# Kernel tuning notes

Hardware: AMD Instinct MI355X
Metric: run time of the kernel (lower is better)

Reference implementation:

```python
import jax, jax.numpy as jnp
import numpy as np

H = 4      # attention heads in HGTConv
DH = 32    # head dim
D = 128    # hidden size (rnn.hidden_size == hidden_size)
PAD = 0    # pad_idx


def setup_inputs() -> dict:
    key = jax.random.key(0)
    ks = jax.random.split(key, 16)
    Na = Np = 50000
    E = 800000
    V = 10000
    L = 8
    s = 0.05  # init scale keeps attention logits stable
    return {
        "tok_author": jax.random.randint(ks[0], (Na, L), 0, V),
        "tok_paper": jax.random.randint(ks[1], (Np, L), 0, V),
        "edge_ap": jax.random.randint(ks[2], (2, E), 0, Np),  # author -> paper
        "edge_pa": jax.random.randint(ks[3], (2, E), 0, Na),  # paper -> author
        "emb": jax.random.normal(ks[4], (V, D)) * s,
        "Wk": jax.random.normal(ks[5], (2, D, D)) * s,
        "Wq": jax.random.normal(ks[6], (2, D, D)) * s,
        "Wv": jax.random.normal(ks[7], (2, D, D)) * s,
        "Watt": jax.random.normal(ks[8], (2, H, DH, DH)) * s,
        "Wmsg": jax.random.normal(ks[9], (2, H, DH, DH)) * s,
        "mu": jnp.ones((2, H), jnp.float32),
        "Wout": jax.random.normal(ks[10], (2, D, D)) * s,
        "lin_w": jax.random.normal(ks[11], (D, D)) * s,
        "lin_b": jnp.zeros((D,), jnp.float32),
    }


def _st_encode(tok, emb):
    # STEncoder stand-in: embedding lookup, pad-masked mean pool, then relu_()
    e = emb[tok]                                   # [N, L, D]
    mask = (tok != PAD).astype(e.dtype)[..., None]  # [N, L, 1]
    pooled = (e * mask).sum(1) / jnp.maximum(mask.sum(1), 1.0)
    return jax.nn.relu(pooled)                     # [N, D]


def _segment_softmax(score, seg, n):
    m = jax.ops.segment_max(score, seg, num_segments=n)
    e = jnp.exp(score - m[seg])
    d = jax.ops.segment_sum(e, seg, num_segments=n)
    return e / (d[seg] + 1e-9)


def _proj(x, W):
    return (x @ W).reshape(x.shape[0], H, DH)


def _rel(k_src, v_src, q_dst, edges, Wa, Wm, mu_r, n_dst):
    # One HGT relation: per-edge key/message transform, segment-softmax attention,
    # scatter-add aggregation into destination nodes.
    src, dst = edges[0], edges[1]
    ke = jnp.einsum('ehd,hdf->ehf', k_src[src], Wa)           # [E, H, DH]
    score = (ke * q_dst[dst]).sum(-1) * mu_r / jnp.sqrt(jnp.float32(DH))  # [E, H]
    alpha = _segment_softmax(score, dst, n_dst)
    me = jnp.einsum('ehd,hdf->ehf', v_src[src], Wm)           # [E, H, DH]
    agg = jax.ops.segment_sum(alpha[..., None] * me, dst, num_segments=n_dst)
    return agg.reshape(n_dst, H * DH)


def reference(tok_author, tok_paper, edge_ap, edge_pa, emb, Wk, Wq, Wv,
              Watt, Wmsg, mu, Wout, lin_w, lin_b):
    # embed + relu per node type
    xa = _st_encode(tok_author, emb)   # [Na, D]
    xp = _st_encode(tok_paper, emb)    # [Np, D]
    Na = xa.shape[0]

    # per-node-type K/Q/V projections (type 0 = author, 1 = paper)
    ka, qa, va = _proj(xa, Wk[0]), _proj(xa, Wq[0]), _proj(xa, Wv[0])
    kp, qp, vp = _proj(xp, Wk[1]), _proj(xp, Wq[1]), _proj(xp, Wv[1])

    # only the 'author' node type feeds the output head, so we only need the
    # paper->author relation's aggregation (rel index 1)
    agg_a = _rel(kp, vp, qa, edge_pa, Watt[1], Wmsg[1], mu[1], Na)
    out_a = jax.nn.gelu(agg_a) @ Wout[0] + xa   # target-type linear + skip

    return out_a @ lin_w + lin_b
```

## Files before the change

kernel.cpp:

```cpp
#include <hip/hip_runtime.h>
#include <math.h>

#define L 8
#define FP8_SCALE 512.0f
#define FP8_INV   0.001953125f

typedef unsigned int  u32;
typedef unsigned short u16;
typedef __attribute__((ext_vector_type(8))) short bf16x8;
typedef __attribute__((ext_vector_type(4))) float f32x4;
typedef __attribute__((ext_vector_type(2))) float f32x2;

__device__ inline u16 f2bf(float x) {
    u32 u = __float_as_uint(x);
    return (u16)((u + 0x7fffu + ((u >> 16) & 1u)) >> 16);
}
__device__ inline float2 bf2f2(u32 v) {
    float2 r;
    r.x = __uint_as_float(v << 16);
    r.y = __uint_as_float(v & 0xffff0000u);
    return r;
}
__device__ inline float gelu_t(float x) {
    return 0.5f * x * (1.0f + tanhf(0.7978845608028654f *
           (x + 0.044715f * x * x * x)));
}

__device__ inline void conv_emb_body(int bid, int tid,
    const float* __restrict__ emb, u32* __restrict__ emb_bf, int n2)
{
    int i = bid * 256 + tid;
    if (i >= n2) return;
    float2 e = *(const float2*)(emb + (size_t)i * 2);
    emb_bf[i] = ((u32)f2bf(e.y) << 16) | (u32)f2bf(e.x);
}

__device__ inline void hist_body8(int bid, int tid,
    const int* __restrict__ dstI, int* __restrict__ deg,
    int* __restrict__ rank, int E, int stride)
{
    int e0 = bid * 256 + tid;
    int d[8], r[8];
#pragma unroll
    for (int j = 0; j < 8; ++j) {
        int e = e0 + j * stride;
        d[j] = (e < E) ? dstI[e] : -1;
    }
#pragma unroll
    for (int j = 0; j < 8; ++j)
        r[j] = (d[j] >= 0) ? atomicAdd(&deg[d[j]], 1) : 0;
#pragma unroll
    for (int j = 0; j < 8; ++j) {
        int e = e0 + j * stride;
        if (d[j] >= 0) rank[e] = r[j];
    }
}

__device__ inline void fold_body(int bid, int tid,
    const float* __restrict__ Wk1, const float* __restrict__ Wq0,
    const float* __restrict__ Wv1, const float* __restrict__ Watt1,
    const float* __restrict__ Wmsg1, const float* __restrict__ Wout0,
    const float* __restrict__ lin_w,
    u16* __restrict__ wkaT, u16* __restrict__ wvmT,
    u16* __restrict__ wqT, u16* __restrict__ w1T, u16* __restrict__ lwT)
{
    int id = bid * 256 + tid;
    int which = id >> 14;
    int idx = id & 16383;
    int col = idx & 127;
    int k = idx >> 7;
    if (which == 0) {
        int h = col >> 5, f = col & 31;
        float s = 0.f;
        for (int d = 0; d < 32; ++d)
            s += Wk1[k * 128 + h * 32 + d] * Watt1[h * 1024 + d * 32 + f];
        wkaT[col * 128 + k] = f2bf(s);
    } else if (which == 1) {
        int h = col >> 5, f = col & 31;
        float s = 0.f;
        for (int d = 0; d < 32; ++d)
            s += Wv1[k * 128 + h * 32 + d] * Wmsg1[h * 1024 + d * 32 + f];
        wvmT[col * 128 + k] = f2bf(s);
    } else if (which == 2) {
        wqT[col * 128 + k] = f2bf(Wq0[k * 128 + col]);
    } else if (which == 3) {
        float s = 0.f;
        for (int d = 0; d < 128; ++d)
            s += Wout0[k * 128 + d] * lin_w[d * 128 + col];
        w1T[col * 128 + k] = f2bf(s);
    } else {
        lwT[col * 128 + k] = f2bf(lin_w[k * 128 + col]);
    }
}

__device__ inline void scan_local_body(int bid, int tid,
    const int* __restrict__ deg, int* __restrict__ locpref,
    int* __restrict__ blocksum, int Na)
{
    __shared__ int lds[256];
    int base = bid * 1024 + tid * 4;
    int4 v = {0, 0, 0, 0};
    if (base + 3 < Na) {
        v = *(const int4*)(deg + base);
    } else {
        if (base + 0 < Na) v.x = deg[base + 0];
        if (base + 1 < Na) v.y = deg[base + 1];
        if (base + 2 < Na) v.z = deg[base + 2];
        if (base + 3 < Na) v.w = deg[base + 3];
    }
    int tot = v.x + v.y + v.z + v.w;
    lds[tid] = tot;
    __syncthreads();
    for (int off = 1; off < 256; off <<= 1) {
        int u = (tid >= off) ? lds[tid - off] : 0;
        __syncthreads();
        lds[tid] += u;
        __syncthreads();
    }
    int excl = lds[tid] - tot;
    if (base < Na) {
        int4 o;
        o.x = excl;
        o.y = excl + v.x;
        o.z = o.y + v.y;
        o.w = o.z + v.z;
        if (base + 3 < Na) *(int4*)(locpref + base) = o;
        else {
            locpref[base] = o.x;
            if (base + 1 < Na) locpref[base + 1] = o.y;
            if (base + 2 < Na) locpref[base + 2] = o.z;
        }
    }
    if (tid == 255) blocksum[bid] = lds[255];
}

__device__ inline void encode_body(int bid, int tid,
    const int* __restrict__ tok_a, const int* __restrict__ tok_p,
    const uint2* __restrict__ emb_bf2,
    uint2* __restrict__ xa2, uint2* __restrict__ xp2, int Na, int Ntot)
{
    int i = bid * 256 + tid;
    int n = i >> 5, q = i & 31;
    if (n >= Ntot) return;
    const int* tok = (n < Na) ? (tok_a + (size_t)n * L)
                              : (tok_p + (size_t)(n - Na) * L);
    int4 t0 = *(const int4*)tok;
    int4 t1 = *(const int4*)(tok + 4);
    int tt[8] = {t0.x, t0.y, t0.z, t0.w, t1.x, t1.y, t1.z, t1.w};
    float ax = 0.f, ay = 0.f, az = 0.f, aw = 0.f;
    int cnt = 0;
#pragma unroll
    for (int l = 0; l < L; ++l) {
        int t = tt[l];
        if (t != 0) {
            cnt++;
            uint2 e = emb_bf2[(size_t)t * 32 + q];
            float2 e0 = bf2f2(e.x), e1 = bf2f2(e.y);
            ax += e0.x; ay += e0.y; az += e1.x; aw += e1.y;
        }
    }
    float dn = 1.0f / fmaxf((float)cnt, 1.0f);
    ax = fmaxf(ax * dn, 0.f); ay = fmaxf(ay * dn, 0.f);
    az = fmaxf(az * dn, 0.f); aw = fmaxf(aw * dn, 0.f);
    uint2 o;
    o.x = ((u32)f2bf(ay) << 16) | (u32)f2bf(ax);
    o.y = ((u32)f2bf(aw) << 16) | (u32)f2bf(az);
    if (n < Na) xa2[(size_t)n * 32 + q] = o;
    else        xp2[(size_t)(n - Na) * 32 + q] = o;
}

__device__ inline void scatter_body16(int bid, int tid,
    const int* __restrict__ srcI, const int* __restrict__ dstI,
    const int* __restrict__ rank, const int* __restrict__ rowptr,
    int* __restrict__ csrc, int E, int stride)
{
    int e0 = bid * 256 + tid;
    int d[16], s[16], r[16];
#pragma unroll
    for (int j = 0; j < 16; ++j) {
        int e = e0 + j * stride;
        d[j] = (e < E) ? dstI[e] : -1;
        s[j] = (e < E) ? srcI[e] : 0;
        r[j] = (e < E) ? rank[e] : 0;
    }
    int base[16];
#pragma unroll
    for (int j = 0; j < 16; ++j)
        base[j] = (d[j] >= 0) ? rowptr[d[j]] : 0;
#pragma unroll
    for (int j = 0; j < 16; ++j)
        if (d[j] >= 0) csrc[base[j] + r[j]] = s[j];
}

__global__ __launch_bounds__(256) void k_prep(
    const float* emb, u32* emb_bf, int n2,
    const int* dstI, int* deg, int* rank, int E, int Bhist8, int stride,
    const float* Wk1, const float* Wq0, const float* Wv1,
    const float* Watt1, const float* Wmsg1, const float* Wout0,
    const float* lin_w, u16* wkaT, u16* wvmT, u16* wqT, u16* w1T, u16* lwT,
    int Bfold)
{
    int b = blockIdx.x, t = threadIdx.x;
    if (b < Bhist8)               hist_body8(b, t, dstI, deg, rank, E, stride);
    else if (b < Bhist8 + Bfold)  fold_body(b - Bhist8, t, Wk1, Wq0, Wv1,
                                      Watt1, Wmsg1, Wout0, lin_w,
                                      wkaT, wvmT, wqT, w1T, lwT);
    else conv_emb_body(b - Bhist8 - Bfold, t, emb, emb_bf, n2);
}

__global__ __launch_bounds__(256) void k_scan_enc(
    const int* deg, int* locpref, int* blocksum, int Na, int BscanL,
    const int* tok_a, const int* tok_p, const uint2* emb_bf2,
    uint2* xa2, uint2* xp2, int Ntot)
{
    int b = blockIdx.x, t = threadIdx.x;
    if (b < BscanL) scan_local_body(b, t, deg, locpref, blocksum, Na);
    else encode_body(b - BscanL, t, tok_a, tok_p, emb_bf2, xa2, xp2, Na, Ntot);
}

__global__ __launch_bounds__(256) void k_final(
    const int* __restrict__ locpref, const int* __restrict__ blocksum,
    int* __restrict__ rowptr, int nb, int Na)
{
    __shared__ int lds[256];
    __shared__ int excl[256];
    int t = threadIdx.x;
    int s = (t < nb) ? blocksum[t] : 0;
    lds[t] = s;
    __syncthreads();
    for (int off = 1; off < 256; off <<= 1) {
        int u = (t >= off) ? lds[t - off] : 0;
        __syncthreads();
        lds[t] += u;
        __syncthreads();
    }
    excl[t] = lds[t] - s;
    __syncthreads();
    int i = blockIdx.x * 256 + t;
    if (i < Na)
        rowptr[i] = locpref[i] + excl[i >> 10];
    if (blockIdx.x == 0 && t == 0)
        rowptr[Na] = lds[nb - 1];
}

__global__ __launch_bounds__(256) void k_scat_proj(
    const int* srcI, const int* dstI, const int* rank, const int* rowptr,
    int* csrc, int E, int Bscat16, int stride,
    const u16* __restrict__ xa, const u16* __restrict__ xp,
    const u16* __restrict__ wqT, const u16* __restrict__ wkaT,
    const u16* __restrict__ wvmT,
    u16* __restrict__ qa, u32* __restrict__ km8, int Na, int Np, int gba,
    int Bproj)
{
    int b = blockIdx.x, t = threadIdx.x;
    if (b % 3 == 0) {
        int sb = b / 3;
        if (sb < Bscat16)
            scatter_body16(sb, t, srcI, dstI, rank, rowptr, csrc, E, stride);
        return;
    }
    int pb = (b / 3) * 2 + (b % 3 - 1);
    if (pb >= Bproj) return;

    int wave = t >> 6;
    int l = t & 63;
    int x = l & 15;
    int kb = (l >> 4) * 8;

    if (pb < gba) {
        int rbase = pb * 64 + wave * 16;
        int arow = rbase + x;
        if (arow >= Na) arow = Na - 1;
        bf16x8 af[4];
#pragma unroll
        for (int ks = 0; ks < 4; ++ks)
            af[ks] = *(const bf16x8*)(xa + (size_t)arow * 128 + ks * 32 + kb);
        f32x4 acc[8];
#pragma unroll
        for (int ct = 0; ct < 8; ++ct) acc[ct] = (f32x4){0.f, 0.f, 0.f, 0.f};
#pragma unroll
        for (int ks = 0; ks < 4; ++ks)
#pragma unroll
            for (int ct = 0; ct < 8; ++ct) {
                bf16x8 bf = *(const bf16x8*)(wqT + (size_t)(ct * 16 + x) * 128 + ks * 32 + kb);
                acc[ct] = __builtin_amdgcn_mfma_f32_16x16x32_bf16(af[ks], bf, acc[ct], 0, 0, 0);
            }
        int srow = rbase + ((l >> 4) << 2);
#pragma unroll
        for (int ct = 0; ct < 8; ++ct) {
            int col = ct * 16 + x;
#pragma unroll
            for (int r = 0; r < 4; ++r)
                if (srow + r < Na)
                    qa[(size_t)(srow + r) * 128 + col] = f2bf(acc[ct][r]);
        }
    } else {
        int b2 = pb - gba;
        int rbase = b2 * 64 + wave * 16;
        int arow = rbase + x;
        if (arow >= Np) arow = Np - 1;
        bf16x8 af[4];
#pragma unroll
        for (int ks = 0; ks < 4; ++ks)
            af[ks] = *(const bf16x8*)(xp + (size_t)arow * 128 + ks * 32 + kb);
        f32x4 kacc[8], macc[8];
#pragma unroll
        for (int ct = 0; ct < 8; ++ct) {
            kacc[ct] = (f32x4){0.f, 0.f, 0.f, 0.f};
            macc[ct] = (f32x4){0.f, 0.f, 0.f, 0.f};
        }
#pragma unroll
        for (int ks = 0; ks < 4; ++ks)
#pragma unroll
            for (int ct = 0; ct < 8; ++ct) {
                bf16x8 bk = *(const bf16x8*)(wkaT + (size_t)(ct * 16 + x) * 128 + ks * 32 + kb);
                kacc[ct] = __builtin_amdgcn_mfma_f32_16x16x32_bf16(af[ks], bk, kacc[ct], 0, 0, 0);
            }
#pragma unroll
        for (int ks = 0; ks < 4; ++ks)
#pragma unroll
            for (int ct = 0; ct < 8; ++ct) {
                bf16x8 bm = *(const bf16x8*)(wvmT + (size_t)(ct * 16 + x) * 128 + ks * 32 + kb);
                macc[ct] = __builtin_amdgcn_mfma_f32_16x16x32_bf16(af[ks], bm, macc[ct], 0, 0, 0);
            }
        int srow = rbase + ((l >> 4) << 2);
#pragma unroll
        for (int ct = 0; ct < 8; ++ct) {
#pragma unroll
            for (int r = 0; r < 4; ++r) {
                float k0 = kacc[ct][r] * FP8_SCALE;
                float k1 = __shfl_xor(k0, 1);
                float m0 = macc[ct][r] * FP8_SCALE;
                float m1 = __shfl_xor(m0, 1);
                if (!(x & 1) && (srow + r) < Np) {
                    int pk = __builtin_amdgcn_cvt_pk_fp8_f32(k0, k1, 0, false);
                    pk = __builtin_amdgcn_cvt_pk_fp8_f32(m0, m1, pk, true);
                    km8[(size_t)(srow + r) * 64 + ct * 8 + (x >> 1)] = (u32)pk;
                }
            }
        }
    }
}

__device__ inline void e_acc(u32 km, float2 qf, float muh,
                             float& dsum, float& a0, float& a1)
{
    f32x2 kf = __builtin_amdgcn_cvt_pk_f32_fp8(km, false);
    f32x2 mf = __builtin_amdgcn_cvt_pk_f32_fp8(km, true);
    float p = kf.x * qf.x + kf.y * qf.y;
    p += __shfl_xor(p, 1, 16);
    p += __shfl_xor(p, 2, 16);
    p += __shfl_xor(p, 4, 16);
    p += __shfl_xor(p, 8, 16);
    float ev = __expf(p * muh);
    dsum += ev; a0 += ev * mf.x; a1 += ev * mf.y;
}

__global__ __launch_bounds__(256) void csr_agg(
    const u32* __restrict__ km8, const u32* __restrict__ qap,
    const int* __restrict__ rowptr, const int* __restrict__ csrc,
    const float* __restrict__ mu1, u32* __restrict__ gagg, int Na)
{
    int dst = blockIdx.x * 4 + (threadIdx.x >> 6);
    if (dst >= Na) return;
    int lane = threadIdx.x & 63;
    int h = lane >> 4;
    float muh = mu1[h] * 0.17677669529663689f * FP8_INV;
    float2 qf = bf2f2(qap[(size_t)dst * 64 + lane]);

    float a0 = 0.f, a1 = 0.f, dsum = 0.f;
    int beg = rowptr[dst], end = rowptr[dst + 1];

    int i = beg;
    for (; i + 8 <= end; i += 8) {
        int s[8];
        u32 km[8];
#pragma unroll
        for (int j = 0; j < 8; ++j) s[j] = csrc[i + j];
#pragma unroll
        for (int j = 0; j < 8; ++j) km[j] = km8[(size_t)s[j] * 64 + lane];
#pragma unroll
        for (int j = 0; j < 8; ++j) e_acc(km[j], qf, muh, dsum, a0, a1);
    }
    for (; i + 4 <= end; i += 4) {
        int s0 = csrc[i], s1 = csrc[i + 1], s2 = csrc[i + 2], s3 = csrc[i + 3];
        u32 km0 = km8[(size_t)s0 * 64 + lane];
        u32 km1 = km8[(size_t)s1 * 64 + lane];
        u32 km2 = km8[(size_t)s2 * 64 + lane];
        u32 km3 = km8[(size_t)s3 * 64 + lane];
        e_acc(km0, qf, muh, dsum, a0, a1);
        e_acc(km1, qf, muh, dsum, a0, a1);
        e_acc(km2, qf, muh, dsum, a0, a1);
        e_acc(km3, qf, muh, dsum, a0, a1);
    }
    for (; i < end; ++i) {
        u32 km0 = km8[(size_t)csrc[i] * 64 + lane];
        e_acc(km0, qf, muh, dsum, a0, a1);
    }
    float dn = dsum + 1e-9f;
    a0 = gelu_t(a0 / dn * FP8_INV);
    a1 = gelu_t(a1 / dn * FP8_INV);
    gagg[(size_t)dst * 64 + lane] = ((u32)f2bf(a1) << 16) | (u32)f2bf(a0);
}

__global__ __launch_bounds__(256) void mfma_out(
    const u16* __restrict__ A0, const u16* __restrict__ WT0,
    const u16* __restrict__ A1, const u16* __restrict__ WT1,
    const float* __restrict__ bias, float* __restrict__ Y, int N)
{
    int wave = threadIdx.x >> 6;
    int l = threadIdx.x & 63;
    int rbase = blockIdx.x * 64 + wave * 16;
    int arow = rbase + (l & 15);
    if (arow >= N) arow = N - 1;
    int kb = (l >> 4) * 8;

    f32x4 acc[8];
#pragma unroll
    for (int ct = 0; ct < 8; ++ct) acc[ct] = (f32x4){0.f, 0.f, 0.f, 0.f};

    for (int w = 0; w < 2; ++w) {
        const u16* A  = w ? A1 : A0;
        const u16* WT = w ? WT1 : WT0;
        bf16x8 af[4];
#pragma unroll
        for (int ks = 0; ks < 4; ++ks)
            af[ks] = *(const bf16x8*)(A + (size_t)arow * 128 + ks * 32 + kb);
#pragma unroll
        for (int ks = 0; ks < 4; ++ks) {
#pragma unroll
            for (int ct = 0; ct < 8; ++ct) {
                bf16x8 bf = *(const bf16x8*)(WT + (size_t)(ct * 16 + (l & 15)) * 128 + ks * 32 + kb);
                acc[ct] = __builtin_amdgcn_mfma_f32_16x16x32_bf16(af[ks], bf, acc[ct], 0, 0, 0);
            }
        }
    }
    int srow = rbase + ((l >> 4) << 2);
#pragma unroll
    for (int ct = 0; ct < 8; ++ct) {
        int col = ct * 16 + (l & 15);
        float b = bias[col];
#pragma unroll
        for (int r = 0; r < 4; ++r) {
            if (srow + r < N)
                Y[(size_t)(srow + r) * 128 + col] = acc[ct][r] + b;
        }
    }
}

extern "C" void kernel_launch(void* const* d_in, const int* in_sizes, int n_in,
                              void* d_out, int out_size, void* d_ws, size_t ws_size,
                              hipStream_t stream)
{
    const int*   tok_a   = (const int*)d_in[0];
    const int*   tok_p   = (const int*)d_in[1];
    const int*   edge_pa = (const int*)d_in[3];
    const float* emb     = (const float*)d_in[4];
    const float* Wk      = (const float*)d_in[5];
    const float* Wq      = (const float*)d_in[6];
    const float* Wv      = (const float*)d_in[7];
    const float* Watt    = (const float*)d_in[8];
    const float* Wmsg    = (const float*)d_in[9];
    const float* mu      = (const float*)d_in[10];
    const float* Wout    = (const float*)d_in[11];
    const float* lin_w   = (const float*)d_in[12];
    const float* lin_b   = (const float*)d_in[13];

    int Na = in_sizes[0] / L;
    int Np = in_sizes[1] / L;
    int E  = in_sizes[3] / 2;
    int V  = in_sizes[4] / 128;
    float* out = (float*)d_out;

    u16* xa      = (u16*)d_ws;
    u16* qa      = xa + (size_t)Na * 128;
    u16* xp      = qa + (size_t)Na * 128;
    u16* gagg    = xp + (size_t)Np * 128;
    u16* emb_bf  = gagg + (size_t)Na * 128;
    u32* km8     = (u32*)(emb_bf + (size_t)V * 128);
    int* deg     = (int*)(km8 + (size_t)Np * 64);
    int* locpref = deg + Na;
    int* rowptr  = locpref + Na;
    int* csrc    = rowptr + Na + 2;
    int* blocksum= csrc + E;
    u16* wkaT    = (u16*)(blocksum + 256);
    u16* wvmT    = wkaT + 16384;
    u16* wqT     = wvmT + 16384;
    u16* w1T     = wqT + 16384;
    u16* lwT     = w1T + 16384;
    int* rank    = (int*)gagg;

    const int* e_src = edge_pa;
    const int* e_dst = edge_pa + E;

    int n2emb   = V * 64;
    int Bconv   = (n2emb + 255) / 256;
    int Bfold   = (5 * 16384) / 256;
    int Bhist8  = (E + 2047) / 2048;
    int hstride = Bhist8 * 256;
    int nb      = (Na + 1023) / 1024;
    int Ntot    = Na + Np;
    int Benc    = ((size_t)Ntot * 32 + 255) / 256;
    int BscanF  = (Na + 255) / 256;
    int gba     = (Na + 63) / 64;
    int gbp     = (Np + 63) / 64;
    int Bproj   = gba + gbp;
    int Bscat16 = (E + 4095) / 4096;
    int sstride = Bscat16 * 256;

    (void)hipMemsetAsync(deg, 0, (size_t)Na * sizeof(int), stream);

    k_prep<<<Bhist8 + Bfold + Bconv, 256, 0, stream>>>(
        emb, (u32*)emb_bf, n2emb,
        e_dst, deg, rank, E, Bhist8, hstride,
        Wk + 16384, Wq, Wv + 16384, Watt + 4096, Wmsg + 4096, Wout, lin_w,
        wkaT, wvmT, wqT, w1T, lwT, Bfold);

    k_scan_enc<<<nb + Benc, 256, 0, stream>>>(
        deg, locpref, blocksum, Na, nb,
        tok_a, tok_p, (const uint2*)emb_bf, (uint2*)xa, (uint2*)xp, Ntot);

    k_final<<<BscanF, 256, 0, stream>>>(locpref, blocksum, rowptr, nb, Na);

    int Gunit = (Bscat16 > (Bproj + 1) / 2) ? Bscat16 : (Bproj + 1) / 2;
    k_scat_proj<<<3 * Gunit, 256, 0, stream>>>(
        e_src, e_dst, rank, rowptr, csrc, E, Bscat16, sstride,
        xa, xp, wqT, wkaT, wvmT, qa, km8, Na, Np, gba, Bproj);

    csr_agg<<<(Na + 3) / 4, 256, 0, stream>>>(
        km8, (const u32*)qa, rowptr, csrc, mu + 4, (u32*)gagg, Na);

    mfma_out<<<gba, 256, 0, stream>>>(gagg, w1T, xa, lwT, lin_b, out, Na);
}
```

Baseline: 218.7 us.

## Regroup fused launches: zero+conv, hist+fold+encode, standalone scan; halve scatter batch

Replaces the memset with a zero-fill body fused into the embedding-conversion launch. Moves the token encoder into the histogram/fold launch so it overlaps with the atomic histogram instead of the scan, and makes the local scan its own small kernel. Scatter now handles 8 edges per thread instead of 16, which doubles scatter blocks to balance against the projection blocks in the interleaved grid. The kernel count stays the same; the aim is better balance of work across launches and fewer critical-path dependencies.

```diff
diff --git a/kernel.cpp b/kernel.cpp
--- a/kernel.cpp
+++ b/kernel.cpp
@@ -24,6 +24,12 @@
 __device__ inline float gelu_t(float x) {
     return 0.5f * x * (1.0f + tanhf(0.7978845608028654f *
            (x + 0.044715f * x * x * x)));
+}
+
+__device__ inline void zero_body(int bid, int tid, int* __restrict__ deg, int Na)
+{
+    int i = bid * 256 + tid;
+    if (i < Na) deg[i] = 0;
 }
 
 __device__ inline void conv_emb_body(int bid, int tid,
@@ -93,12 +99,98 @@
     }
 }
 
-__device__ inline void scan_local_body(int bid, int tid,
+__device__ inline void encode_body(int bid, int tid,
+    const int* __restrict__ tok_a, const int* __restrict__ tok_p,
+    const uint2* __restrict__ emb_bf2,
+    uint2* __restrict__ xa2, uint2* __restrict__ xp2, int Na, int Ntot)
+{
+    int i = bid * 256 + tid;
+    int n = i >> 5, q = i & 31;
+    if (n >= Ntot) return;
+    const int* tok = (n < Na) ? (tok_a + (size_t)n * L)
+                              : (tok_p + (size_t)(n - Na) * L);
+    int4 t0 = *(const int4*)tok;
+    int4 t1 = *(const int4*)(tok + 4);
+    int tt[8] = {t0.x, t0.y, t0.z, t0.w, t1.x, t1.y, t1.z, t1.w};
+    float ax = 0.f, ay = 0.f, az = 0.f, aw = 0.f;
+    int cnt = 0;
+#pragma unroll
+    for (int l = 0; l < L; ++l) {
+        int t = tt[l];
+        if (t != 0) {
+            cnt++;
+            uint2 e = emb_bf2[(size_t)t * 32 + q];
+            float2 e0 = bf2f2(e.x), e1 = bf2f2(e.y);
+            ax += e0.x; ay += e0.y; az += e1.x; aw += e1.y;
+        }
+    }
+    float dn = 1.0f / fmaxf((float)cnt, 1.0f);
+    ax = fmaxf(ax * dn, 0.f); ay = fmaxf(ay * dn, 0.f);
+    az = fmaxf(az * dn, 0.f); aw = fmaxf(aw * dn, 0.f);
+    uint2 o;
+    o.x = ((u32)f2bf(ay) << 16) | (u32)f2bf(ax);
+    o.y = ((u32)f2bf(aw) << 16) | (u32)f2bf(az);
+    if (n < Na) xa2[(size_t)n * 32 + q] = o;
+    else        xp2[(size_t)(n - Na) * 32 + q] = o;
+}
+
+__device__ inline void scatter_body8(int bid, int tid,
+    const int* __restrict__ srcI, const int* __restrict__ dstI,
+    const int* __restrict__ rank, const int* __restrict__ rowptr,
+    int* __restrict__ csrc, int E, int stride)
+{
+    int e0 = bid * 256 + tid;
+    int d[8], s[8], r[8];
+#pragma unroll
+    for (int j = 0; j < 8; ++j) {
+        int e = e0 + j * stride;
+        d[j] = (e < E) ? dstI[e] : -1;
+        s[j] = (e < E) ? srcI[e] : 0;
+        r[j] = (e < E) ? rank[e] : 0;
+    }
+    int base[8];
+#pragma unroll
+    for (int j = 0; j < 8; ++j)
+        base[j] = (d[j] >= 0) ? rowptr[d[j]] : 0;
+#pragma unroll
+    for (int j = 0; j < 8; ++j)
+        if (d[j] >= 0) csrc[base[j] + r[j]] = s[j];
+}
+
+__global__ __launch_bounds__(256) void k_zero_conv(
+    int* deg, int Na, int Bzero,
+    const float* emb, u32* emb_bf, int n2)
+{
+    int b = blockIdx.x, t = threadIdx.x;
+    if (b < Bzero) zero_body(b, t, deg, Na);
+    else           conv_emb_body(b - Bzero, t, emb, emb_bf, n2);
+}
+
+__global__ __launch_bounds__(256) void k_prep(
+    const int* dstI, int* deg, int* rank, int E, int Bhist8, int stride,
+    const float* Wk1, const float* Wq0, const float* Wv1,
+    const float* Watt1, const float* Wmsg1, const float* Wout0,
+    const float* lin_w, u16* wkaT, u16* wvmT, u16* wqT, u16* w1T, u16* lwT,
+    int Bfold,
+    const int* tok_a, const int* tok_p, const uint2* emb_bf2,
+    uint2* xa2, uint2* xp2, int Na, int Ntot)
+{
+    int b = blockIdx.x, t = threadIdx.x;
+    if (b < Bhist8)               hist_body8(b, t, dstI, deg, rank, E, stride);
+    else if (b < Bhist8 + Bfold)  fold_body(b - Bhist8, t, Wk1, Wq0, Wv1,
+                                      Watt1, Wmsg1, Wout0, lin_w,
+                                      wkaT, wvmT, wqT, w1T, lwT);
+    else encode_body(b - Bhist8 - Bfold, t, tok_a, tok_p, emb_bf2,
+                     xa2, xp2, Na, Ntot);
+}
+
+__global__ __launch_bounds__(256) void k_scan(
     const int* __restrict__ deg, int* __restrict__ locpref,
     int* __restrict__ blocksum, int Na)
 {
     __shared__ int lds[256];
-    int base = bid * 1024 + tid * 4;
+    int tid = threadIdx.x;
+    int base = blockIdx.x * 1024 + tid * 4;
     int4 v = {0, 0, 0, 0};
     if (base + 3 < Na) {
         v = *(const int4*)(deg + base);
@@ -131,91 +223,7 @@
             if (base + 2 < Na) locpref[base + 2] = o.z;
         }
     }
-    if (tid == 255) blocksum[bid] = lds[255];
-}
-
-__device__ inline void encode_body(int bid, int tid,
-    const int* __restrict__ tok_a, const int* __restrict__ tok_p,
-    const uint2* __restrict__ emb_bf2,
-    uint2* __restrict__ xa2, uint2* __restrict__ xp2, int Na, int Ntot)
-{
-    int i = bid * 256 + tid;
-    int n = i >> 5, q = i & 31;
-    if (n >= Ntot) return;
-    const int* tok = (n < Na) ? (tok_a + (size_t)n * L)
-                              : (tok_p + (size_t)(n - Na) * L);
-    int4 t0 = *(const int4*)tok;
-    int4 t1 = *(const int4*)(tok + 4);
-    int tt[8] = {t0.x, t0.y, t0.z, t0.w, t1.x, t1.y, t1.z, t1.w};
-    float ax = 0.f, ay = 0.f, az = 0.f, aw = 0.f;
-    int cnt = 0;
-#pragma unroll
-    for (int l = 0; l < L; ++l) {
-        int t = tt[l];
-        if (t != 0) {
-            cnt++;
-            uint2 e = emb_bf2[(size_t)t * 32 + q];
-            float2 e0 = bf2f2(e.x), e1 = bf2f2(e.y);
-            ax += e0.x; ay += e0.y; az += e1.x; aw += e1.y;
-        }
-    }
-    float dn = 1.0f / fmaxf((float)cnt, 1.0f);
-    ax = fmaxf(ax * dn, 0.f); ay = fmaxf(ay * dn, 0.f);
-    az = fmaxf(az * dn, 0.f); aw = fmaxf(aw * dn, 0.f);
-    uint2 o;
-    o.x = ((u32)f2bf(ay) << 16) | (u32)f2bf(ax);
-    o.y = ((u32)f2bf(aw) << 16) | (u32)f2bf(az);
-    if (n < Na) xa2[(size_t)n * 32 + q] = o;
-    else        xp2[(size_t)(n - Na) * 32 + q] = o;
-}
-
-__device__ inline void scatter_body16(int bid, int tid,
-    const int* __restrict__ srcI, const int* __restrict__ dstI,
-    const int* __restrict__ rank, const int* __restrict__ rowptr,
-    int* __restrict__ csrc, int E, int stride)
-{
-    int e0 = bid * 256 + tid;
-    int d[16], s[16], r[16];
-#pragma unroll
-    for (int j = 0; j < 16; ++j) {
-        int e = e0 + j * stride;
-        d[j] = (e < E) ? dstI[e] : -1;
-        s[j] = (e < E) ? srcI[e] : 0;
-        r[j] = (e < E) ? rank[e] : 0;
-    }
-    int base[16];
-#pragma unroll
-    for (int j = 0; j < 16; ++j)
-        base[j] = (d[j] >= 0) ? rowptr[d[j]] : 0;
-#pragma unroll
-    for (int j = 0; j < 16; ++j)
-        if (d[j] >= 0) csrc[base[j] + r[j]] = s[j];
-}
-
-__global__ __launch_bounds__(256) void k_prep(
-    const float* emb, u32* emb_bf, int n2,
-    const int* dstI, int* deg, int* rank, int E, int Bhist8, int stride,
-    const float* Wk1, const float* Wq0, const float* Wv1,
-    const float* Watt1, const float* Wmsg1, const float* Wout0,
-    const float* lin_w, u16* wkaT, u16* wvmT, u16* wqT, u16* w1T, u16* lwT,
-    int Bfold)
-{
-    int b = blockIdx.x, t = threadIdx.x;
-    if (b < Bhist8)               hist_body8(b, t, dstI, deg, rank, E, stride);
-    else if (b < Bhist8 + Bfold)  fold_body(b - Bhist8, t, Wk1, Wq0, Wv1,
-                                      Watt1, Wmsg1, Wout0, lin_w,
-                                      wkaT, wvmT, wqT, w1T, lwT);
-    else conv_emb_body(b - Bhist8 - Bfold, t, emb, emb_bf, n2);
-}
-
-__global__ __launch_bounds__(256) void k_scan_enc(
-    const int* deg, int* locpref, int* blocksum, int Na, int BscanL,
-    const int* tok_a, const int* tok_p, const uint2* emb_bf2,
-    uint2* xa2, uint2* xp2, int Ntot)
-{
-    int b = blockIdx.x, t = threadIdx.x;
-    if (b < BscanL) scan_local_body(b, t, deg, locpref, blocksum, Na);
-    else encode_body(b - BscanL, t, tok_a, tok_p, emb_bf2, xa2, xp2, Na, Ntot);
+    if (tid == 255) blocksum[blockIdx.x] = lds[255];
 }
 
 __global__ __launch_bounds__(256) void k_final(
@@ -245,7 +253,7 @@
 
 __global__ __launch_bounds__(256) void k_scat_proj(
     const int* srcI, const int* dstI, const int* rank, const int* rowptr,
-    int* csrc, int E, int Bscat16, int stride,
+    int* csrc, int E, int Bscat8, int stride,
     const u16* __restrict__ xa, const u16* __restrict__ xp,
     const u16* __restrict__ wqT, const u16* __restrict__ wkaT,
     const u16* __restrict__ wvmT,
@@ -255,8 +263,8 @@
     int b = blockIdx.x, t = threadIdx.x;
     if (b % 3 == 0) {
         int sb = b / 3;
-        if (sb < Bscat16)
-            scatter_body16(sb, t, srcI, dstI, rank, rowptr, csrc, E, stride);
+        if (sb < Bscat8)
+            scatter_body8(sb, t, srcI, dstI, rank, rowptr, csrc, E, stride);
         return;
     }
     int pb = (b / 3) * 2 + (b % 3 - 1);
@@ -495,6 +503,7 @@
 
     int n2emb   = V * 64;
     int Bconv   = (n2emb + 255) / 256;
+    int Bzero   = (Na + 255) / 256;
     int Bfold   = (5 * 16384) / 256;
     int Bhist8  = (E + 2047) / 2048;
     int hstride = Bhist8 * 256;
@@ -505,26 +514,25 @@
     int gba     = (Na + 63) / 64;
     int gbp     = (Np + 63) / 64;
     int Bproj   = gba + gbp;
-    int Bscat16 = (E + 4095) / 4096;
-    int sstride = Bscat16 * 256;
-
-    (void)hipMemsetAsync(deg, 0, (size_t)Na * sizeof(int), stream);
-
-    k_prep<<<Bhist8 + Bfold + Bconv, 256, 0, stream>>>(
-        emb, (u32*)emb_bf, n2emb,
+    int Bscat8  = (E + 2047) / 2048;
+    int sstride = Bscat8 * 256;
+
+    k_zero_conv<<<Bzero + Bconv, 256, 0, stream>>>(
+        deg, Na, Bzero, emb, (u32*)emb_bf, n2emb);
+
+    k_prep<<<Bhist8 + Bfold + Benc, 256, 0, stream>>>(
         e_dst, deg, rank, E, Bhist8, hstride,
         Wk + 16384, Wq, Wv + 16384, Watt + 4096, Wmsg + 4096, Wout, lin_w,
-        wkaT, wvmT, wqT, w1T, lwT, Bfold);
-
-    k_scan_enc<<<nb + Benc, 256, 0, stream>>>(
-        deg, locpref, blocksum, Na, nb,
-        tok_a, tok_p, (const uint2*)emb_bf, (uint2*)xa, (uint2*)xp, Ntot);
+        wkaT, wvmT, wqT, w1T, lwT, Bfold,
+        tok_a, tok_p, (const uint2*)emb_bf, (uint2*)xa, (uint2*)xp, Na, Ntot);
+
+    k_scan<<<nb, 256, 0, stream>>>(deg, locpref, blocksum, Na);
 
     k_final<<<BscanF, 256, 0, stream>>>(locpref, blocksum, rowptr, nb, Na);
 
-    int Gunit = (Bscat16 > (Bproj + 1) / 2) ? Bscat16 : (Bproj + 1) / 2;
+    int Gunit = (Bscat8 > (Bproj + 1) / 2) ? Bscat8 : (Bproj + 1) / 2;
     k_scat_proj<<<3 * Gunit, 256, 0, stream>>>(
-        e_src, e_dst, rank, rowptr, csrc, E, Bscat16, sstride,
+        e_src, e_dst, rank, rowptr, csrc, E, Bscat8, sstride,
         xa, xp, wqT, wkaT, wvmT, qa, km8, Na, Np, gba, Bproj);
 
     csr_agg<<<(Na + 3) / 4, 256, 0, stream>>>(
```

Result: faster. 205.2 us (-6.2%).
